# Optimization experiments

Measured on AMD Instinct MI355X. Metric: run time of the kernel, lower is better.

Reference implementation:

```python
import jax, jax.numpy as jnp
import numpy as np

B, C, H, W = 2, 64, 64, 64
C2 = C // 2
N = H * W


def conv1x1(x, w, b):
    # x: (B,Cin,H,W), w: (Cout,Cin), b: (Cout,)
    return jnp.einsum('bchw,oc->bohw', x, w) + b[None, :, None, None]


def setup_inputs() -> dict:
    key = jax.random.key(0)
    ks = jax.random.split(key, 20)
    s = 0.05
    d = {
        'x1': jax.random.normal(ks[0], (B, C, H, W), jnp.float32),
        'x2': jax.random.normal(ks[1], (B, C, H, W), jnp.float32),
        'wq1': jax.random.normal(ks[2], (C2, C), jnp.float32) * s,
        'bq1': jax.random.normal(ks[3], (C2,), jnp.float32) * s,
        'wk1': jax.random.normal(ks[4], (C2, C), jnp.float32) * s,
        'bk1': jax.random.normal(ks[5], (C2,), jnp.float32) * s,
        'wv1': jax.random.normal(ks[6], (C2, C), jnp.float32) * s,
        'bv1': jax.random.normal(ks[7], (C2,), jnp.float32) * s,
        'wc1': jax.random.normal(ks[8], (C, C2), jnp.float32) * s,
        'bc1': jax.random.normal(ks[9], (C,), jnp.float32) * s,
        'wq2': jax.random.normal(ks[10], (C2, C), jnp.float32) * s,
        'bq2': jax.random.normal(ks[11], (C2,), jnp.float32) * s,
        'wk2': jax.random.normal(ks[12], (C2, C), jnp.float32) * s,
        'bk2': jax.random.normal(ks[13], (C2,), jnp.float32) * s,
        'wv2': jax.random.normal(ks[14], (C2, C), jnp.float32) * s,
        'bv2': jax.random.normal(ks[15], (C2,), jnp.float32) * s,
        'wc2': jax.random.normal(ks[16], (C, C2), jnp.float32) * s,
        'bc2': jax.random.normal(ks[17], (C,), jnp.float32) * s,
        'gamma1': jax.random.normal(ks[18], (1,), jnp.float32) * 0.5,
        'gamma2': jax.random.normal(ks[19], (1,), jnp.float32) * 0.5,
    }
    return d


def reference(x1, x2, wq1, bq1, wk1, bk1, wv1, bv1, wc1, bc1,
              wq2, bq2, wk2, bk2, wv2, bv2, wc2, bc2, gamma1, gamma2):
    b, c, h, w = x1.shape
    n = h * w
    # branch-1 projections (boundary semantics)
    q1 = jnp.max(conv1x1(x1, wq1, bq1), axis=1).reshape(b, n)          # (B,N) channel-max
    k1 = jnp.max(conv1x1(x1, wk1, bk1).reshape(b, -1, n), axis=1)      # (B,N)
    v1 = conv1x1(x1, wv1, bv1).reshape(b, -1, n)                        # (B,C/2,N)
    # branch-2 projections (field semantics)
    q2 = jnp.mean(conv1x1(x2, wq2, bq2), axis=1).reshape(b, n)         # (B,N) channel-mean
    k2 = jnp.mean(conv1x1(x2, wk2, bk2).reshape(b, -1, n), axis=1)     # (B,N)
    v2 = conv1x1(x2, wv2, bv2).reshape(b, -1, n)                        # (B,C/2,N)
    # energy2 = q1 (B,N,1) @ k2 (B,1,N) outer product; inverted sigmoid gate
    att2 = 1.0 - jax.nn.sigmoid(q1[:, :, None] * k2[:, None, :])        # (B,N,N)
    out1 = jnp.einsum('bck,bmk->bcm', v1, att2).reshape(b, c // 2, h, w)
    out1 = conv1x1(out1, wc2, bc2)
    # energy1 = q2 outer k1; sigmoid gate
    att1 = jax.nn.sigmoid(q2[:, :, None] * k1[:, None, :])              # (B,N,N)
    out2 = jnp.einsum('bck,bmk->bcm', v2, att1).reshape(b, c // 2, h, w)
    out2 = conv1x1(out2, wc1, bc1)
    out1 = x1 + gamma1[0] * out1
    out2 = x2 + gamma2[0] * out2
    return (out1, out2)
```

## Files before the change

### kernel.cpp

```cpp
#include <hip/hip_runtime.h>
#include <hip/hip_bf16.h>

#define NN 4096
#define CC 64
#define C2 32
#define BB 2

#define NSEG   4
#define M_BLK  32
#define KBLK   64
#define KB_ITERS (NN / NSEG / KBLK)

#define WS_Q1 0
#define WS_K1 8192
#define WS_Q2 16384
#define WS_K2 24576
#define WS_V1 32768
#define WS_V2 163840
#define WS_P  294912

typedef __attribute__((address_space(1))) const unsigned int GUI;
typedef __attribute__((address_space(3))) unsigned int LUI;
typedef __attribute__((ext_vector_type(8))) short bf16x8;
typedef __attribute__((ext_vector_type(4))) float f32x4;

__device__ __forceinline__ void glds16(const void* g, void* l) {
    __builtin_amdgcn_global_load_lds((GUI*)g, (LUI*)l, 16, 0, 0);
}

__device__ __forceinline__ unsigned short bf16_rne(float f) {
    union { float f; unsigned u; } x; x.f = f;
    unsigned u = x.u + 0x7fff + ((x.u >> 16) & 1);
    return (unsigned short)(u >> 16);
}
__device__ __forceinline__ unsigned pack2(float a, float b) {
    __hip_bfloat162 h = __float22bfloat162_rn(make_float2(a, b));
    unsigned r; __builtin_memcpy(&r, &h, 4); return r;
}
__device__ __forceinline__ float sigm_e2(float x) {
    return __builtin_amdgcn_rcpf(1.0f + __builtin_amdgcn_exp2f(x));
}

__global__ __launch_bounds__(256) void proj_kernel(
    const float* __restrict__ x1, const float* __restrict__ x2,
    const float* __restrict__ wq1, const float* __restrict__ bq1,
    const float* __restrict__ wk1, const float* __restrict__ bk1,
    const float* __restrict__ wv1, const float* __restrict__ bv1,
    const float* __restrict__ wq2, const float* __restrict__ bq2,
    const float* __restrict__ wk2, const float* __restrict__ bk2,
    const float* __restrict__ wv2, const float* __restrict__ bv2,
    float* __restrict__ ws)
{
    const int ln = threadIdx.x & 63;
    const int og = threadIdx.x >> 6;
    const int n  = blockIdx.x * 64 + ln;
    const int p  = blockIdx.y;
    const int b  = blockIdx.z;

    const float* x; const float* w; const float* bias;
    int mode; float* dstf; unsigned short* dstv;
    switch (p) {
      case 0: x = x1; w = wq1; bias = bq1; mode = 0; dstf = ws + WS_Q1; dstv = 0; break;
      case 1: x = x1; w = wk1; bias = bk1; mode = 0; dstf = ws + WS_K1; dstv = 0; break;
      case 2: x = x1; w = wv1; bias = bv1; mode = 2; dstf = 0; dstv = (unsigned short*)(ws + WS_V1); break;
      case 3: x = x2; w = wq2; bias = bq2; mode = 1; dstf = ws + WS_Q2; dstv = 0; break;
      case 4: x = x2; w = wk2; bias = bk2; mode = 1; dstf = ws + WS_K2; dstv = 0; break;
      default:x = x2; w = wv2; bias = bv2; mode = 2; dstf = 0; dstv = (unsigned short*)(ws + WS_V2); break;
    }

    __shared__ float red[4][C2][64];

    float acc[C2];
    #pragma unroll
    for (int o = 0; o < C2; ++o) acc[o] = 0.0f;

    const float* xb = x + ((size_t)b * CC + og * 16) * NN + n;
    #pragma unroll
    for (int ci = 0; ci < 16; ++ci) {
        const float xv = xb[(size_t)ci * NN];
        #pragma unroll
        for (int o = 0; o < C2; ++o)
            acc[o] += w[o * CC + og * 16 + ci] * xv;
    }
    #pragma unroll
    for (int o = 0; o < C2; ++o) red[og][o][ln] = acc[o];
    __syncthreads();

    float f[8];
    #pragma unroll
    for (int j = 0; j < 8; ++j) {
        const int o = og * 8 + j;
        f[j] = red[0][o][ln] + red[1][o][ln] + red[2][o][ln] + red[3][o][ln]
             + bias[o];
    }

    if (mode == 2) {
        #pragma unroll
        for (int j = 0; j < 8; ++j)
            dstv[((size_t)b * C2 + og * 8 + j) * NN + n] = bf16_rne(f[j]);
    } else {
        float r;
        if (mode == 0) {
            r = f[0];
            #pragma unroll
            for (int j = 1; j < 8; ++j) r = fmaxf(r, f[j]);
        } else {
            r = 0.0f;
            #pragma unroll
            for (int j = 0; j < 8; ++j) r += f[j];
        }
        __syncthreads();
        red[og][0][ln] = r;
        __syncthreads();
        if (og == 0) {
            const float a0 = red[0][0][ln], a1 = red[1][0][ln];
            const float a2 = red[2][0][ln], a3 = red[3][0][ln];
            const float rr = (mode == 0)
                ? fmaxf(fmaxf(a0, a1), fmaxf(a2, a3))
                : (a0 + a1 + a2 + a3) * (1.0f / C2);
            dstf[(size_t)b * NN + n] = rr;
        }
    }
}

__global__ __launch_bounds__(256) void attn_mfma(
    const float* __restrict__ q1, const float* __restrict__ k1,
    const float* __restrict__ q2, const float* __restrict__ k2,
    const unsigned short* __restrict__ v1, const unsigned short* __restrict__ v2,
    float* __restrict__ pout)
{
    __shared__ unsigned short vtile[2][C2 * KBLK];
    __shared__ unsigned short stile[2][M_BLK * KBLK];

    const int tid = threadIdx.x;
    const int wv  = tid >> 6;
    const int ln  = tid & 63;

    const int seg    = blockIdx.y;
    const int z      = blockIdx.z;
    const int branch = z & 1;
    const int b      = z >> 1;
    const int m0     = blockIdx.x * M_BLK;
    const int kstart = seg * (NN / NSEG);

    const float* q; const float* kv; const unsigned short* vbf; float sl2e;
    if (branch == 0) { q = q1; kv = k2; vbf = v1; sl2e =  1.44269504089f; }
    else             { q = q2; kv = k1; vbf = v2; sl2e = -1.44269504089f; }

    const int sm = tid & 31;
    const int sc = tid >> 5;
    const float qs = q[(size_t)b * NN + m0 + sm] * sl2e;
    const float* kvb = kv + (size_t)b * NN;

    f32x4 acc[2];
    #pragma unroll
    for (int mt = 0; mt < 2; ++mt) acc[mt] = (f32x4){0.f, 0.f, 0.f, 0.f};

    const int vc = tid >> 3;
    const int vs = tid & 7;
    const unsigned short* vsrc0 = vbf + (size_t)(b * C2 + vc) * NN
                                + ((vs ^ (vc & 7)) << 3);

    auto sigPackWrite = [&](int buf, float4 ka, float4 kb4) {
        float s[8];
        s[0] = sigm_e2(qs * ka.x);  s[1] = sigm_e2(qs * ka.y);
        s[2] = sigm_e2(qs * ka.z);  s[3] = sigm_e2(qs * ka.w);
        s[4] = sigm_e2(qs * kb4.x); s[5] = sigm_e2(qs * kb4.y);
        s[6] = sigm_e2(qs * kb4.z); s[7] = sigm_e2(qs * kb4.w);

        uint4 w;
        w.x = pack2(s[0], s[1]); w.y = pack2(s[2], s[3]);
        w.z = pack2(s[4], s[5]); w.w = pack2(s[6], s[7]);

        char* srow = (char*)stile[buf] + sm * 128;
        *(uint4*)(srow + ((sc ^ (sm & 7)) << 4)) = w;
    };

    glds16(vsrc0 + kstart, (char*)vtile[0] + tid * 16);
    {
        const float* kvp = kvb + kstart + sc * 8;
        sigPackWrite(0, *(const float4*)(kvp), *(const float4*)(kvp + 4));
    }
    asm volatile("s_waitcnt vmcnt(0)" ::: "memory");
    __syncthreads();

    const int ct  = wv & 1;
    const int ks  = wv >> 1;
    const int col = (ks << 2) + (ln >> 4);
    const int ac  = ct * 16 + (ln & 15);

    for (int kb = 0; kb < KB_ITERS; ++kb) {
        const int cur = kb & 1;
        const bool more = (kb + 1 < KB_ITERS);

        float4 ka, kb4;
        if (more) {
            glds16(vsrc0 + kstart + (kb + 1) * KBLK,
                   (char*)vtile[cur ^ 1] + tid * 16);
            const float* kvp = kvb + kstart + (kb + 1) * KBLK + sc * 8;
            ka  = *(const float4*)(kvp);
            kb4 = *(const float4*)(kvp + 4);
        }

        const bf16x8 af = *(const bf16x8*)((const char*)vtile[cur]
                          + ac * 128 + ((col ^ (ac & 7)) << 4));
        #pragma unroll
        for (int mt = 0; mt < 2; ++mt) {
            const int bm = mt * 16 + (ln & 15);
            const bf16x8 bfr = *(const bf16x8*)((const char*)stile[cur]
                               + bm * 128 + ((col ^ (bm & 7)) << 4));
            acc[mt] = __builtin_amdgcn_mfma_f32_16x16x32_bf16(af, bfr, acc[mt], 0, 0, 0);
        }

        if (more) sigPackWrite(cur ^ 1, ka, kb4);

        asm volatile("s_waitcnt vmcnt(0)" ::: "memory");
        __syncthreads();
    }

    float* red = (float*)stile;
    if (wv >= 2) {
        #pragma unroll
        for (int mt = 0; mt < 2; ++mt)
            *(f32x4*)&red[((wv - 2) * 2 + mt) * 256 + ln * 4] = acc[mt];
    }
    __syncthreads();
    if (wv < 2) {
        const size_t obase = (((size_t)(branch * NSEG + seg) * BB + b) * C2) * NN;
        #pragma unroll
        for (int mt = 0; mt < 2; ++mt) {
            const f32x4 o = *(const f32x4*)&red[(wv * 2 + mt) * 256 + ln * 4];
            acc[mt].x += o.x; acc[mt].y += o.y; acc[mt].z += o.z; acc[mt].w += o.w;
            #pragma unroll
            for (int j = 0; j < 4; ++j) {
                const int c = wv * 16 + (ln >> 4) * 4 + j;
                const int m = m0 + mt * 16 + (ln & 15);
                pout[obase + (size_t)c * NN + m] = acc[mt][j];
            }
        }
    }
}

__global__ __launch_bounds__(256) void conv_kernel(
    const float* __restrict__ x1, const float* __restrict__ x2,
    const float* __restrict__ wc1, const float* __restrict__ bc1,
    const float* __restrict__ wc2, const float* __restrict__ bc2,
    const float* __restrict__ g1,  const float* __restrict__ g2,
    const float* __restrict__ p,   float* __restrict__ out)
{
    const int m      = blockIdx.x * 256 + threadIdx.x;
    const int co0    = blockIdx.y * 8;
    const int b      = blockIdx.z >> 1;
    const int branch = blockIdx.z & 1;

    const float* w; const float* bias; const float* x; float gamma; float* o;
    if (branch == 0) { w = wc2; bias = bc2; x = x1; gamma = g1[0]; o = out; }
    else             { w = wc1; bias = bc1; x = x2; gamma = g2[0]; o = out + (size_t)BB * CC * NN; }

    float s[C2];
    #pragma unroll
    for (int c = 0; c < C2; ++c) s[c] = 0.0f;

    #pragma unroll 1
    for (int seg = 0; seg < NSEG; ++seg) {
        const float* sb = p + (((size_t)(branch * NSEG + seg) * BB + b) * C2) * NN + m;
        #pragma unroll
        for (int c = 0; c < C2; ++c)
            s[c] += sb[(size_t)c * NN];
    }

    #pragma unroll
    for (int co = co0; co < co0 + 8; ++co) {
        float a = bias[co];
        #pragma unroll
        for (int c = 0; c < C2; ++c)
            a += w[co * C2 + c] * s[c];
        const size_t idx = ((size_t)b * CC + co) * NN + m;
        o[idx] = x[idx] + gamma * a;
    }
}

extern "C" void kernel_launch(void* const* d_in, const int* in_sizes, int n_in,
                              void* d_out, int out_size, void* d_ws, size_t ws_size,
                              hipStream_t stream)
{
    const float* x1  = (const float*)d_in[0];
    const float* x2  = (const float*)d_in[1];
    const float* wq1 = (const float*)d_in[2];
    const float* bq1 = (const float*)d_in[3];
    const float* wk1 = (const float*)d_in[4];
    const float* bk1 = (const float*)d_in[5];
    const float* wv1 = (const float*)d_in[6];
    const float* bv1 = (const float*)d_in[7];
    const float* wc1 = (const float*)d_in[8];
    const float* bc1 = (const float*)d_in[9];
    const float* wq2 = (const float*)d_in[10];
    const float* bq2 = (const float*)d_in[11];
    const float* wk2 = (const float*)d_in[12];
    const float* bk2 = (const float*)d_in[13];
    const float* wv2 = (const float*)d_in[14];
    const float* bv2 = (const float*)d_in[15];
    const float* wc2 = (const float*)d_in[16];
    const float* bc2 = (const float*)d_in[17];
    const float* g1  = (const float*)d_in[18];
    const float* g2  = (const float*)d_in[19];

    float* ws  = (float*)d_ws;
    float* out = (float*)d_out;

    proj_kernel<<<dim3(NN / 64, 6, BB), 256, 0, stream>>>(
        x1, x2, wq1, bq1, wk1, bk1, wv1, bv1,
        wq2, bq2, wk2, bk2, wv2, bv2, ws);

    const float* q1 = ws + WS_Q1; const float* k1 = ws + WS_K1;
    const float* q2 = ws + WS_Q2; const float* k2 = ws + WS_K2;
    const unsigned short* v1 = (const unsigned short*)(ws + WS_V1);
    const unsigned short* v2 = (const unsigned short*)(ws + WS_V2);
    float* pp = ws + WS_P;

    attn_mfma<<<dim3(NN / M_BLK, NSEG, BB * 2), 256, 0, stream>>>(
        q1, k1, q2, k2, v1, v2, pp);

    conv_kernel<<<dim3(NN / 256, 8, BB * 2), 256, 0, stream>>>(
        x1, x2, wc1, bc1, wc2, bc2, g1, g2, pp, out);
}
```

Before: 49.83 us.

## Fuse output 1x1 conv into attention kernel and drop key-split partials

New measurement: 61.35 us. 1.23x slower.

```diff
diff --git a/kernel.cpp b/kernel.cpp
--- a/kernel.cpp
+++ b/kernel.cpp
@@ -6,10 +6,9 @@
 #define C2 32
 #define BB 2
 
-#define NSEG   4
 #define M_BLK  32
 #define KBLK   64
-#define KB_ITERS (NN / NSEG / KBLK)
+#define KB_ITERS (NN / KBLK)
 
 #define WS_Q1 0
 #define WS_K1 8192
@@ -17,7 +16,6 @@
 #define WS_K2 24576
 #define WS_V1 32768
 #define WS_V2 163840
-#define WS_P  294912
 
 typedef __attribute__((address_space(1))) const unsigned int GUI;
 typedef __attribute__((address_space(3))) unsigned int LUI;
@@ -127,7 +125,11 @@
     const float* __restrict__ q1, const float* __restrict__ k1,
     const float* __restrict__ q2, const float* __restrict__ k2,
     const unsigned short* __restrict__ v1, const unsigned short* __restrict__ v2,
-    float* __restrict__ pout)
+    const float* __restrict__ x1,  const float* __restrict__ x2,
+    const float* __restrict__ wc1, const float* __restrict__ bc1,
+    const float* __restrict__ wc2, const float* __restrict__ bc2,
+    const float* __restrict__ g1,  const float* __restrict__ g2,
+    float* __restrict__ out)
 {
     __shared__ unsigned short vtile[2][C2 * KBLK];
     __shared__ unsigned short stile[2][M_BLK * KBLK];
@@ -136,12 +138,10 @@
     const int wv  = tid >> 6;
     const int ln  = tid & 63;
 
-    const int seg    = blockIdx.y;
-    const int z      = blockIdx.z;
+    const int z      = blockIdx.y;
     const int branch = z & 1;
     const int b      = z >> 1;
     const int m0     = blockIdx.x * M_BLK;
-    const int kstart = seg * (NN / NSEG);
 
     const float* q; const float* kv; const unsigned short* vbf; float sl2e;
     if (branch == 0) { q = q1; kv = k2; vbf = v1; sl2e =  1.44269504089f; }
@@ -176,9 +176,9 @@
         *(uint4*)(srow + ((sc ^ (sm & 7)) << 4)) = w;
     };
 
-    glds16(vsrc0 + kstart, (char*)vtile[0] + tid * 16);
+    glds16(vsrc0, (char*)vtile[0] + tid * 16);
     {
-        const float* kvp = kvb + kstart + sc * 8;
+        const float* kvp = kvb + sc * 8;
         sigPackWrite(0, *(const float4*)(kvp), *(const float4*)(kvp + 4));
     }
     asm volatile("s_waitcnt vmcnt(0)" ::: "memory");
@@ -195,9 +195,9 @@
 
         float4 ka, kb4;
         if (more) {
-            glds16(vsrc0 + kstart + (kb + 1) * KBLK,
+            glds16(vsrc0 + (kb + 1) * KBLK,
                    (char*)vtile[cur ^ 1] + tid * 16);
-            const float* kvp = kvb + kstart + (kb + 1) * KBLK + sc * 8;
+            const float* kvp = kvb + (kb + 1) * KBLK + sc * 8;
             ka  = *(const float4*)(kvp);
             kb4 = *(const float4*)(kvp + 4);
         }
@@ -225,8 +225,8 @@
             *(f32x4*)&red[((wv - 2) * 2 + mt) * 256 + ln * 4] = acc[mt];
     }
     __syncthreads();
+    float* s_lds = (float*)vtile;
     if (wv < 2) {
-        const size_t obase = (((size_t)(branch * NSEG + seg) * BB + b) * C2) * NN;
         #pragma unroll
         for (int mt = 0; mt < 2; ++mt) {
             const f32x4 o = *(const f32x4*)&red[(wv * 2 + mt) * 256 + ln * 4];
@@ -234,48 +234,34 @@
             #pragma unroll
             for (int j = 0; j < 4; ++j) {
                 const int c = wv * 16 + (ln >> 4) * 4 + j;
-                const int m = m0 + mt * 16 + (ln & 15);
-                pout[obase + (size_t)c * NN + m] = acc[mt][j];
+                const int m = mt * 16 + (ln & 15);
+                s_lds[c * M_BLK + m] = acc[mt][j];
             }
         }
     }
-}
-
-__global__ __launch_bounds__(256) void conv_kernel(
-    const float* __restrict__ x1, const float* __restrict__ x2,
-    const float* __restrict__ wc1, const float* __restrict__ bc1,
-    const float* __restrict__ wc2, const float* __restrict__ bc2,
-    const float* __restrict__ g1,  const float* __restrict__ g2,
-    const float* __restrict__ p,   float* __restrict__ out)
-{
-    const int m      = blockIdx.x * 256 + threadIdx.x;
-    const int co0    = blockIdx.y * 8;
-    const int b      = blockIdx.z >> 1;
-    const int branch = blockIdx.z & 1;
-
-    const float* w; const float* bias; const float* x; float gamma; float* o;
-    if (branch == 0) { w = wc2; bias = bc2; x = x1; gamma = g1[0]; o = out; }
-    else             { w = wc1; bias = bc1; x = x2; gamma = g2[0]; o = out + (size_t)BB * CC * NN; }
-
-    float s[C2];
-    #pragma unroll
-    for (int c = 0; c < C2; ++c) s[c] = 0.0f;
-
-    #pragma unroll 1
-    for (int seg = 0; seg < NSEG; ++seg) {
-        const float* sb = p + (((size_t)(branch * NSEG + seg) * BB + b) * C2) * NN + m;
+    __syncthreads();
+
+    const float* wmat; const float* bias; const float* x; float gamma;
+    float* o;
+    if (branch == 0) { wmat = wc2; bias = bc2; x = x1; gamma = g1[0]; o = out; }
+    else             { wmat = wc1; bias = bc1; x = x2; gamma = g2[0];
+                       o = out + (size_t)BB * CC * NN; }
+
+    const int m  = tid & 31;
+    const int cg = tid >> 5;
+
+    float sv[C2];
+    #pragma unroll
+    for (int c = 0; c < C2; ++c) sv[c] = s_lds[c * M_BLK + m];
+
+    #pragma unroll
+    for (int j = 0; j < 8; ++j) {
+        const int co = cg * 8 + j;
+        float a = bias[co];
         #pragma unroll
         for (int c = 0; c < C2; ++c)
-            s[c] += sb[(size_t)c * NN];
-    }
-
-    #pragma unroll
-    for (int co = co0; co < co0 + 8; ++co) {
-        float a = bias[co];
-        #pragma unroll
-        for (int c = 0; c < C2; ++c)
-            a += w[co * C2 + c] * s[c];
-        const size_t idx = ((size_t)b * CC + co) * NN + m;
+            a += wmat[co * C2 + c] * sv[c];
+        const size_t idx = ((size_t)b * CC + co) * NN + m0 + m;
         o[idx] = x[idx] + gamma * a;
     }
 }
@@ -316,11 +302,8 @@
     const float* q2 = ws + WS_Q2; const float* k2 = ws + WS_K2;
     const unsigned short* v1 = (const unsigned short*)(ws + WS_V1);
     const unsigned short* v2 = (const unsigned short*)(ws + WS_V2);
-    float* pp = ws + WS_P;
-
-    attn_mfma<<<dim3(NN / M_BLK, NSEG, BB * 2), 256, 0, stream>>>(
-        q1, k1, q2, k2, v1, v2, pp);
-
-    conv_kernel<<<dim3(NN / 256, 8, BB * 2), 256, 0, stream>>>(
-        x1, x2, wc1, bc1, wc2, bc2, g1, g2, pp, out);
-}
+
+    attn_mfma<<<dim3(NN / M_BLK, BB * 2), 256, 0, stream>>>(
+        q1, k1, q2, k2, v1, v2,
+        x1, x2, wc1, bc1, wc2, bc2, g1, g2, out);
+}
```
